# Performance work log

Hardware: AMD Instinct MI355X
Metric: run time of the kernel (lower is better)

The kernel has to match this reference:

```python
import jax, jax.numpy as jnp
import numpy as np

B, L, N, C = 32, 12, 2048, 3
D = 64          # embed_dim
TOPK = 8
NK = 16         # n_kernel
TOD = 288
DOW = 7
OUT = 12        # output_len
NLAYER = 3
HS = 3 * D + TOPK * D + D        # spatial_hidden_dim = 768
HT = 4 * D + TOPK * D + D        # temporal_hidden_dim = 832
HC = int(100 * 0.1 * np.log(N / 0.1))  # EmbeddingTrainer bottleneck = 99
EPS = 1e-8


def setup_inputs() -> dict:
    key = jax.random.key(0)
    ks = jax.random.split(key, 20)
    r = lambda i, shape, s=0.02: jax.random.normal(ks[i], shape, jnp.float32) * s
    return dict(
        history_data=jax.random.uniform(ks[0], (B, L, N, C), jnp.float32),
        future_data=jax.random.uniform(ks[1], (B, OUT, N, C), jnp.float32),
        node_emb=r(2, (N, D), 0.1),
        et_w1=r(3, (HC, N)), et_b1=jnp.zeros((HC,), jnp.float32),
        et_w2=r(4, (N, HC)), et_b2=jnp.zeros((N,), jnp.float32),
        tod_emb=r(5, (TOD, D), 0.1), dow_emb=r(6, (DOW, D), 0.1),
        ts_w=r(7, (D, L), 0.1),
        feature_emb=r(8, (NK, D), 0.1),
        kernels=r(9, (NK, L), 0.1),
        sp_w=r(10, (D, HS)), sp_b=jnp.zeros((D,), jnp.float32),
        mlp_w1=r(11, (NLAYER, HT, HT), 0.01), mlp_b1=jnp.zeros((NLAYER, HT), jnp.float32),
        mlp_w2=r(12, (NLAYER, HT, HT), 0.01), mlp_b2=jnp.zeros((NLAYER, HT), jnp.float32),
        treg_w=r(13, (OUT, L), 0.1), treg_b=jnp.zeros((OUT,), jnp.float32),
        sreg_w=r(14, (OUT, HT), 0.02), sreg_b=jnp.zeros((OUT,), jnp.float32),
        daily_data=r(15, (TOD, N), 0.01), weekly_data=r(16, (DOW, N), 0.01),
        w_spatial=jnp.full((N,), 0.5, jnp.float32),
        batch_seen=0, epoch=0, train=1,
    )


def _forward(history_data, future_data, node_emb, et_w1, et_b1, et_w2, et_b2,
             tod_emb, dow_emb, ts_w, feature_emb, kernels, sp_w, sp_b,
             mlp_w1, mlp_b1, mlp_w2, mlp_b2, treg_w, treg_b, sreg_w, sreg_b,
             daily_data, weekly_data, w_spatial):
    x_in = history_data[..., 0]                              # (B,L,N)
    # --- temporal embeddings at last step ---
    tod_idx = (history_data[:, -1, :, 1] * TOD).astype(jnp.int32)   # (B,N)
    dow_idx = (history_data[:, -1, :, 2] * DOW).astype(jnp.int32)
    tid = tod_emb[tod_idx]                                   # (B,N,D)
    diw = dow_emb[dow_idx]
    # --- time-series embedding (1x1 conv over L channels) ---
    ts_emb = jnp.einsum('bln,dl->bdn', x_in, ts_w)           # (B,D,N)
    # --- EmbeddingTrainer: compress/reconstruct along node axis ---
    z = jax.nn.relu(jnp.einsum('nd,hn->dh', node_emb, et_w1) + et_b1)   # (D,HC)
    proj_node = (jnp.einsum('dh,nh->dn', z, et_w2) + et_b2).T           # (N,D)
    # --- NFConnection: cosine correlation node-series vs kernel bank ---
    xn = x_in / (jnp.linalg.norm(x_in, axis=1, keepdims=True) + EPS)
    kn = kernels / (jnp.linalg.norm(kernels, axis=1, keepdims=True) + EPS)
    conn = jnp.einsum('bln,kl->bnk', xn, kn)                 # (B,N,NK)
    c_weight, c_index = jax.lax.top_k(conn, TOPK)            # (B,N,TOPK)
    corr = jax.nn.sigmoid(c_weight)[..., None] * feature_emb[c_index]   # (B,N,TOPK,D)
    corr_ch = corr.reshape(B, N, TOPK * D).transpose(0, 2, 1)           # (B,TOPK*D,N)
    Hinc = jax.nn.one_hot(c_index, NK, dtype=jnp.float32).sum(axis=2)   # (B,N,NK)
    # --- assemble spatial encoder input ---
    node_ch = jnp.broadcast_to(proj_node.T[None], (B, D, N))
    enc_in = jnp.concatenate([ts_emb, node_ch, tid.transpose(0, 2, 1),
                              diw.transpose(0, 2, 1), corr_ch], axis=1)  # (B,HS,N)
    # --- SpatiaEncoder: 1x1 proj + hypergraph message passing ---
    h0 = jax.nn.relu(jnp.einsum('bcn,dc->bdn', enc_in, sp_w) + sp_b[None, :, None])
    deg_e = jnp.maximum(Hinc.sum(axis=1), 1.0)               # (B,NK)
    edge = jnp.einsum('bnk,bdn->bdk', Hinc, h0) / deg_e[:, None, :]
    edge = edge + feature_emb.T[None]                        # add hyperedge (kernel) embeddings
    msg = jnp.einsum('bnk,bdk->bdn', Hinc, edge) / TOPK
    sp_out = h0 + msg + proj_node.T[None]                    # (B,D,N)
    # --- temporal encoder: residual MLP stack ---
    h = jnp.concatenate([enc_in, sp_out], axis=1)            # (B,HT,N)
    for i in range(NLAYER):
        z1 = jax.nn.relu(jnp.einsum('bcn,dc->bdn', h, mlp_w1[i]) + mlp_b1[i][None, :, None])
        h = h + jnp.einsum('bcn,dc->bdn', z1, mlp_w2[i]) + mlp_b2[i][None, :, None]
    forecast_sp = jnp.einsum('bcn,oc->bon', h, sreg_w) + sreg_b[None, :, None]  # (B,OUT,N)
    # --- temporal branch: RevIN + daily/weekly cycle queues ---
    di_b = (history_data[:, :, 0, 1] * TOD).astype(jnp.int32)   # (B,L)
    wi_b = (history_data[:, :, 0, 2] * DOW).astype(jnp.int32)
    mean = x_in.mean(axis=1, keepdims=True)                  # (B,1,N)
    var = jnp.var(x_in, axis=1, keepdims=True, ddof=1) + 1e-5
    xr = (x_in - mean) / jnp.sqrt(var) - (daily_data[di_b] + weekly_data[wi_b])
    forecast_t = jnp.einsum('bln,ol->bon', xr, treg_w) + treg_b[None, :, None]
    di_f = (future_data[:, :, 0, 1] * TOD).astype(jnp.int32)
    wi_f = (future_data[:, :, 0, 2] * DOW).astype(jnp.int32)
    forecast_t = forecast_t + daily_data[di_f] + weekly_data[wi_f]
    forecast_t = forecast_t * jnp.sqrt(var) + mean
    pred = w_spatial[None, None, :] * forecast_sp + (1.0 - w_spatial)[None, None, :] * forecast_t
    return pred[..., None]                                   # (B,OUT,N,1)


def reference(history_data, future_data, node_emb, et_w1, et_b1, et_w2, et_b2,
              tod_emb, dow_emb, ts_w, feature_emb, kernels, sp_w, sp_b,
              mlp_w1, mlp_b1, mlp_w2, mlp_b2, treg_w, treg_b, sreg_w, sreg_b,
              daily_data, weekly_data, w_spatial, batch_seen, epoch, train):
    return _forward(history_data, future_data, node_emb, et_w1, et_b1, et_w2, et_b2,
                    tod_emb, dow_emb, ts_w, feature_emb, kernels, sp_w, sp_b,
                    mlp_w1, mlp_b1, mlp_w2, mlp_b2, treg_w, treg_b, sreg_w, sreg_b,
                    daily_data, weekly_data, w_spatial)
```

## Files before the change

### kernel.cpp

```cpp
#include <hip/hip_runtime.h>
#include <hip/hip_bf16.h>
#include <math.h>

#define BB 32
#define LL 12
#define NN 2048
#define DD 64
#define TOPK 8
#define NKER 16
#define OUTL 12
#define HS 768
#define HT 832
#define HTP 896
#define HCB 99
#define BN (BB*NN)

typedef __attribute__((ext_vector_type(8))) short bf16x8;
typedef __attribute__((ext_vector_type(4))) float f32x4;

#define GLOAD16(gp, lp) __builtin_amdgcn_global_load_lds( \
    (const __attribute__((address_space(1))) unsigned int*)(uintptr_t)(gp), \
    (__attribute__((address_space(3))) unsigned int*)(unsigned int)(uintptr_t)(lp), \
    16, 0, 0)

__global__ __launch_bounds__(256)
void f2b_pad_kernel(const float* __restrict__ x, __hip_bfloat16* __restrict__ y,
                    int rows, int cols, int prows) {
    int i = blockIdx.x * 256 + threadIdx.x;
    if (i >= prows * cols) return;
    int r = i / cols;
    y[i] = __float2bfloat16((r < rows) ? x[i] : 0.f);
}

__global__ __launch_bounds__(64)
void et_z_kernel(const float* __restrict__ node_emb, const float* __restrict__ w1,
                 const float* __restrict__ b1, float* __restrict__ z) {
    int hh = blockIdx.x;
    int d  = threadIdx.x;
    float acc = 0.f;
    for (int nn = 0; nn < NN; ++nn)
        acc += node_emb[nn*DD + d] * w1[(size_t)hh*NN + nn];
    acc += b1[hh];
    z[d*HCB + hh] = fmaxf(acc, 0.f);
}

__global__ __launch_bounds__(64)
void et_proj_kernel(const float* __restrict__ z, const float* __restrict__ w2,
                    const float* __restrict__ b2, float* __restrict__ proj) {
    int nn = blockIdx.x;
    int d  = threadIdx.x;
    float acc = 0.f;
    for (int hh = 0; hh < HCB; ++hh)
        acc += z[d*HCB + hh] * w2[nn*HCB + hh];
    proj[nn*DD + d] = acc + b2[nn];
}

__global__ __launch_bounds__(64)
void prep_kernel(const float* __restrict__ hist, const float* __restrict__ proj,
                 const float* __restrict__ tod_emb, const float* __restrict__ dow_emb,
                 const float* __restrict__ ts_w, const float* __restrict__ feat_emb,
                 const float* __restrict__ kern, __hip_bfloat16* __restrict__ h,
                 int* __restrict__ cidx, unsigned int* __restrict__ mask) {
    const int tok = blockIdx.x;
    const int b = tok >> 11, n = tok & (NN-1);
    const int lane = threadIdx.x;
    __shared__ float xs[LL];
    __shared__ float conn_s[NKER];
    __shared__ int   idx_s[TOPK];
    __shared__ float w_s[TOPK];

    if (lane < LL)
        xs[lane] = hist[((size_t)(b*LL + lane) * NN + n) * 3];
    __syncthreads();

    if (lane < NKER) {
        float xn = 0.f;
        #pragma unroll
        for (int l = 0; l < LL; ++l) xn += xs[l]*xs[l];
        xn = sqrtf(xn) + 1e-8f;
        float kn = 0.f;
        #pragma unroll
        for (int l = 0; l < LL; ++l) { float kv = kern[lane*LL + l]; kn += kv*kv; }
        kn = sqrtf(kn) + 1e-8f;
        float dot = 0.f;
        #pragma unroll
        for (int l = 0; l < LL; ++l) dot += (xs[l]/xn) * (kern[lane*LL + l]/kn);
        conn_s[lane] = dot;
    }
    __syncthreads();

    if (lane == 0) {
        float c[NKER];
        #pragma unroll
        for (int k = 0; k < NKER; ++k) c[k] = conn_s[k];
        unsigned int mk = 0;
        for (int j = 0; j < TOPK; ++j) {
            float best = -1e30f; int bi = 0;
            #pragma unroll
            for (int k = 0; k < NKER; ++k)
                if (c[k] > best) { best = c[k]; bi = k; }
            idx_s[j] = bi;
            w_s[j] = 1.f / (1.f + expf(-best));
            c[bi] = -1e30f;
            mk |= (1u << bi);
            cidx[(size_t)tok*TOPK + j] = bi;
        }
        mask[tok] = mk;
    }
    __syncthreads();

    const int d = lane;
    float ts = 0.f;
    #pragma unroll
    for (int l = 0; l < LL; ++l) ts += xs[l] * ts_w[d*LL + l];
    size_t base = (size_t)tok * HT;
    h[base + d] = __float2bfloat16(ts);
    h[base + DD + d] = __float2bfloat16(proj[n*DD + d]);
    size_t last = ((size_t)(b*LL + (LL-1)) * NN + n) * 3;
    int ti = (int)(hist[last + 1] * 288.f);
    int wi = (int)(hist[last + 2] * 7.f);
    h[base + 2*DD + d] = __float2bfloat16(tod_emb[ti*DD + d]);
    h[base + 3*DD + d] = __float2bfloat16(dow_emb[wi*DD + d]);
    #pragma unroll
    for (int j = 0; j < TOPK; ++j)
        h[base + 4*DD + j*DD + d] = __float2bfloat16(w_s[j] * feat_emb[idx_s[j]*DD + d]);
}

template<int RELU, int ACCUM, int CF32, int NCOLS>
__global__ __launch_bounds__(256)
void gemm128(const unsigned short* __restrict__ A, int lda,
             const unsigned short* __restrict__ W, int ldb,
             const float* __restrict__ bias,
             void* __restrict__ Cp, int ldc, int K, int ntiles) {
    __shared__ __align__(16) unsigned short As[128*64];
    __shared__ __align__(16) unsigned short Bs[128*64];

    int nwg = gridDim.x, bid = blockIdx.x;
    int q = nwg >> 3, r = nwg & 7;
    int xcd = bid & 7, idx = bid >> 3;
    int swz = ((xcd < r) ? xcd*(q+1) : r*(q+1) + (xcd-r)*q) + idx;
    const long long m0 = (long long)(swz / ntiles) * 128;
    const int n0 = (swz % ntiles) * 128;

    const int tid = threadIdx.x;
    const int wave = tid >> 6, lane = tid & 63;
    const int wr = wave >> 1, wc = wave & 1;
    const int l15 = lane & 15, l4 = lane >> 4;

    const int srow = tid >> 3;
    const int gc = ((tid & 7) ^ ((tid >> 3) & 7)) * 8;
    const unsigned short* ag = A + (m0 + srow) * (long long)lda + gc;
    const unsigned short* bg = W + (long long)(n0 + srow) * ldb + gc;

    f32x4 acc[4][4] = {};

    for (int k0 = 0; k0 < K; k0 += 64) {
        #pragma unroll
        for (int qq = 0; qq < 4; ++qq) {
            GLOAD16(ag + k0 + (long long)qq*32*lda, &As[(qq*256 + tid)*8]);
            GLOAD16(bg + k0 + (long long)qq*32*ldb, &Bs[(qq*256 + tid)*8]);
        }
        __syncthreads();
        #pragma unroll
        for (int kh = 0; kh < 2; ++kh) {
            bf16x8 af[4], bf[4];
            #pragma unroll
            for (int i = 0; i < 4; ++i) {
                int ra = wr*64 + i*16 + l15;
                af[i] = *(const bf16x8*)&As[ra*64 + (((kh*4 + l4) ^ (ra & 7)) * 8)];
            }
            #pragma unroll
            for (int j = 0; j < 4; ++j) {
                int rb = wc*64 + j*16 + l15;
                bf[j] = *(const bf16x8*)&Bs[rb*64 + (((kh*4 + l4) ^ (rb & 7)) * 8)];
            }
            #pragma unroll
            for (int i = 0; i < 4; ++i)
                #pragma unroll
                for (int j = 0; j < 4; ++j)
                    acc[i][j] = __builtin_amdgcn_mfma_f32_16x16x32_bf16(af[i], bf[j], acc[i][j], 0, 0, 0);
        }
        __syncthreads();
    }

    float* Cf = (float*)Cp;
    __hip_bfloat16* Cb = (__hip_bfloat16*)Cp;
    #pragma unroll
    for (int i = 0; i < 4; ++i) {
        #pragma unroll
        for (int j = 0; j < 4; ++j) {
            int col = n0 + wc*64 + j*16 + l15;
            if (col < NCOLS) {
                float bv = bias[col];
                #pragma unroll
                for (int rg = 0; rg < 4; ++rg) {
                    long long row = m0 + wr*64 + i*16 + l4*4 + rg;
                    float v = acc[i][j][rg] + bv;
                    if (RELU) v = fmaxf(v, 0.f);
                    if (CF32) {
                        Cf[row*ldc + col] = v;
                    } else {
                        if (ACCUM) v += __bfloat162float(Cb[row*ldc + col]);
                        Cb[row*ldc + col] = __float2bfloat16(v);
                    }
                }
            }
        }
    }
}

__global__ __launch_bounds__(256)
void edge_kernel(const float* __restrict__ h0, const unsigned int* __restrict__ mask,
                 const float* __restrict__ feat_emb, float* __restrict__ edge) {
    int b = blockIdx.x >> 4, k = blockIdx.x & 15;
    int g = threadIdx.x >> 6, d = threadIdx.x & 63;
    __shared__ float accs[4][64];
    __shared__ int cnts[4];
    float acc = 0.f; int cnt = 0;
    size_t tb = (size_t)b * NN;
    #pragma unroll 4
    for (int nn = g; nn < NN; nn += 4) {
        unsigned int bit = (mask[tb + nn] >> k) & 1u;
        acc += (float)bit * h0[(tb + nn)*DD + d];
        cnt += (int)bit;
    }
    accs[g][d] = acc;
    if (d == 0) cnts[g] = cnt;
    __syncthreads();
    if (g == 0) {
        float a = accs[0][d] + accs[1][d] + accs[2][d] + accs[3][d];
        int c = cnts[0] + cnts[1] + cnts[2] + cnts[3];
        edge[((size_t)b*NKER + k)*DD + d] = a / fmaxf((float)c, 1.f) + feat_emb[k*DD + d];
    }
}

__global__ __launch_bounds__(256)
void msg_kernel(const float* __restrict__ h0, const float* __restrict__ edge,
                const int* __restrict__ cidx, const float* __restrict__ proj,
                __hip_bfloat16* __restrict__ h) {
    __shared__ float eS[NKER*DD];
    int t0 = blockIdx.x * 4;
    int b = t0 >> 11;
    for (int i = threadIdx.x; i < NKER*DD; i += 256) eS[i] = edge[(size_t)b*NKER*DD + i];
    __syncthreads();
    int g = threadIdx.x >> 6, lane = threadIdx.x & 63;
    int tok = t0 + g, n = tok & (NN-1);
    float m = 0.f;
    #pragma unroll
    for (int j = 0; j < TOPK; ++j)
        m += eS[cidx[(size_t)tok*TOPK + j]*DD + lane];
    float sp = h0[(size_t)tok*DD + lane] + m*0.125f + proj[n*DD + lane];
    h[(size_t)tok*HT + HS + lane] = __float2bfloat16(sp);
}

__global__ __launch_bounds__(256)
void temporal_kernel(const float* __restrict__ hist, const float* __restrict__ fut,
                     const float* __restrict__ daily, const float* __restrict__ weekly,
                     const float* __restrict__ treg_w, const float* __restrict__ treg_b,
                     float* __restrict__ outp) {
    __shared__ int s_di[LL], s_wi[LL], s_df[OUTL], s_wf[OUTL];
    __shared__ float s_tw[OUTL*LL], s_tb[OUTL];
    int tid = threadIdx.x;
    int tok = blockIdx.x * 256 + tid;
    int b = tok >> 11, n = tok & (NN-1);
    if (tid < LL) {
        size_t hb = ((size_t)(b*LL + tid) * NN) * 3;
        s_di[tid] = (int)(hist[hb + 1] * 288.f);
        s_wi[tid] = (int)(hist[hb + 2] * 7.f);
        size_t fb = ((size_t)(b*OUTL + tid) * NN) * 3;
        s_df[tid] = (int)(fut[fb + 1] * 288.f);
        s_wf[tid] = (int)(fut[fb + 2] * 7.f);
        s_tb[tid] = treg_b[tid];
    }
    if (tid < OUTL*LL) s_tw[tid] = treg_w[tid];
    __syncthreads();
    float x[LL];
    float mean = 0.f;
    #pragma unroll
    for (int l = 0; l < LL; ++l) {
        x[l] = hist[((size_t)(b*LL + l) * NN + n) * 3];
        mean += x[l];
    }
    mean *= (1.f/12.f);
    float ss = 0.f;
    #pragma unroll
    for (int l = 0; l < LL; ++l) { float dd = x[l]-mean; ss += dd*dd; }
    float sd = sqrtf(ss*(1.f/11.f) + 1e-5f);
    float xr[LL];
    #pragma unroll
    for (int l = 0; l < LL; ++l)
        xr[l] = (x[l]-mean)/sd - daily[(size_t)s_di[l]*NN + n] - weekly[(size_t)s_wi[l]*NN + n];
    #pragma unroll
    for (int o = 0; o < OUTL; ++o) {
        float f = s_tb[o];
        #pragma unroll
        for (int l = 0; l < LL; ++l) f += xr[l]*s_tw[o*LL + l];
        f += daily[(size_t)s_df[o]*NN + n] + weekly[(size_t)s_wf[o]*NN + n];
        f = f*sd + mean;
        outp[((size_t)b*OUTL + o)*NN + n] = f;
    }
}

__global__ __launch_bounds__(256)
void final_kernel(const __hip_bfloat16* __restrict__ h, const float* __restrict__ sreg_w,
                  const float* __restrict__ sreg_b, const float* __restrict__ w_sp,
                  float* __restrict__ outp) {
    int g = threadIdx.x >> 6, lane = threadIdx.x & 63;
    int tok = blockIdx.x*4 + g;
    int b = tok >> 11, n = tok & (NN-1);
    float acc[OUTL];
    #pragma unroll
    for (int o = 0; o < OUTL; ++o) acc[o] = 0.f;
    size_t base = (size_t)tok * HT;
    for (int c = lane; c < HT; c += 64) {
        float hv = __bfloat162float(h[base + c]);
        #pragma unroll
        for (int o = 0; o < OUTL; ++o) acc[o] += hv * sreg_w[o*HT + c];
    }
    #pragma unroll
    for (int o = 0; o < OUTL; ++o) {
        #pragma unroll
        for (int s = 32; s >= 1; s >>= 1)
            acc[o] += __shfl_xor(acc[o], s, 64);
    }
    float v = 0.f;
    #pragma unroll
    for (int o = 0; o < OUTL; ++o) if (lane == o) v = acc[o] + sreg_b[o];
    if (lane < OUTL) {
        size_t oi = ((size_t)b*OUTL + lane)*NN + n;
        float t = outp[oi];
        float w = w_sp[n];
        outp[oi] = w*v + (1.f-w)*t;
    }
}

extern "C" void kernel_launch(void* const* d_in, const int* in_sizes, int n_in,
                              void* d_out, int out_size, void* d_ws, size_t ws_size,
                              hipStream_t stream) {
    const float* hist    = (const float*)d_in[0];
    const float* fut     = (const float*)d_in[1];
    const float* node_emb= (const float*)d_in[2];
    const float* et_w1   = (const float*)d_in[3];
    const float* et_b1   = (const float*)d_in[4];
    const float* et_w2   = (const float*)d_in[5];
    const float* et_b2   = (const float*)d_in[6];
    const float* tod_emb = (const float*)d_in[7];
    const float* dow_emb = (const float*)d_in[8];
    const float* ts_w    = (const float*)d_in[9];
    const float* feat    = (const float*)d_in[10];
    const float* kern    = (const float*)d_in[11];
    const float* sp_w    = (const float*)d_in[12];
    const float* sp_b    = (const float*)d_in[13];
    const float* mlp_w1  = (const float*)d_in[14];
    const float* mlp_b1  = (const float*)d_in[15];
    const float* mlp_w2  = (const float*)d_in[16];
    const float* mlp_b2  = (const float*)d_in[17];
    const float* treg_w  = (const float*)d_in[18];
    const float* treg_b  = (const float*)d_in[19];
    const float* sreg_w  = (const float*)d_in[20];
    const float* sreg_b  = (const float*)d_in[21];
    const float* daily   = (const float*)d_in[22];
    const float* weekly  = (const float*)d_in[23];
    const float* w_sp    = (const float*)d_in[24];
    float* out = (float*)d_out;

    char* ws = (char*)d_ws;
    __hip_bfloat16* h    = (__hip_bfloat16*)(ws);
    float*          h0   = (float*)(ws + 109051904ULL);
    float*          proj = (float*)(ws + 125829120ULL);
    float*          zet  = (float*)(ws + 126353408ULL);
    float*          edge = (float*)(ws + 126386176ULL);
    int*            cidx = (int*)  (ws + 126517248ULL);
    unsigned int*   mask = (unsigned int*)(ws + 128614400ULL);
    __hip_bfloat16* spwb = (__hip_bfloat16*)(ws + 128876544ULL);
    __hip_bfloat16* w1b  = (__hip_bfloat16*)(ws + 129073152ULL);
    __hip_bfloat16* w2b  = (__hip_bfloat16*)(ws + 133545984ULL);
    const size_t z1_off = 138018816ULL;
    __hip_bfloat16* z1   = (__hip_bfloat16*)(ws + z1_off);

    long long avail = (ws_size > z1_off) ? (long long)(ws_size - z1_off) : 0;
    long long chunk = (avail / (HT*2)) & ~127LL;
    if (chunk > BN) chunk = BN;
    if (chunk < 128) chunk = 128;

    f2b_pad_kernel<<<(128*HS + 255)/256, 256, 0, stream>>>(sp_w, spwb, 64, HS, 128);
    for (int i = 0; i < 3; ++i) {
        f2b_pad_kernel<<<(HTP*HT + 255)/256, 256, 0, stream>>>(
            mlp_w1 + (size_t)i*HT*HT, w1b + (size_t)i*HTP*HT, HT, HT, HTP);
        f2b_pad_kernel<<<(HTP*HT + 255)/256, 256, 0, stream>>>(
            mlp_w2 + (size_t)i*HT*HT, w2b + (size_t)i*HTP*HT, HT, HT, HTP);
    }

    et_z_kernel  <<<HCB, 64, 0, stream>>>(node_emb, et_w1, et_b1, zet);
    et_proj_kernel<<<NN, 64, 0, stream>>>(zet, et_w2, et_b2, proj);
    prep_kernel  <<<BN, 64, 0, stream>>>(hist, proj, tod_emb, dow_emb, ts_w, feat, kern,
                                         h, cidx, mask);
    gemm128<1,0,1,64><<<BN/128, 256, 0, stream>>>(
        (const unsigned short*)h, HT, (const unsigned short*)spwb, HS, sp_b, h0, DD, HS, 1);
    edge_kernel  <<<BB*NKER, 256, 0, stream>>>(h0, mask, feat, edge);
    msg_kernel   <<<BN/4, 256, 0, stream>>>(h0, edge, cidx, proj, h);
    for (int i = 0; i < 3; ++i) {
        for (long long ms = 0; ms < BN; ms += chunk) {
            long long mm = (BN - ms < chunk) ? (BN - ms) : chunk;
            int grid = (int)(mm/128) * (HTP/128);
            gemm128<1,0,0,HT><<<grid, 256, 0, stream>>>(
                (const unsigned short*)(h + ms*HT), HT,
                (const unsigned short*)(w1b + (size_t)i*HTP*HT), HT,
                mlp_b1 + i*HT, z1, HT, HT, HTP/128);
            gemm128<0,1,0,HT><<<grid, 256, 0, stream>>>(
                (const unsigned short*)z1, HT,
                (const unsigned short*)(w2b + (size_t)i*HTP*HT), HT,
                mlp_b2 + i*HT, h + ms*HT, HT, HT, HTP/128);
        }
    }
    temporal_kernel<<<BN/256, 256, 0, stream>>>(hist, fut, daily, weekly, treg_w, treg_b, out);
    final_kernel <<<BN/4, 256, 0, stream>>>(h, sreg_w, sreg_b, w_sp, out);
}
```

Before: 1.217 ms.

## Use double-buffered 256x256 tile GEMM for the temporal MLP layers

Adds a 512-thread gemm256 kernel with 256x256 output tiles and a two-stage LDS double buffer. It uses explicit vmcnt waits so the next K-slice loads while the MFMAs run on the current one. The six MLP GEMMs switch to it, with weights padded to 1024 rows, and the chunk size is aligned to 256. The aim is more data reuse per tile and less exposed global-load latency, at the cost of about 19% wasted MFMA work on padded columns (832 of 1024) and a 128KB LDS footprint that likely limits each CU to one workgroup.

After: 1.333 ms. 9.5% more time.

```diff
diff --git a/kernel.cpp b/kernel.cpp
--- a/kernel.cpp
+++ b/kernel.cpp
@@ -11,7 +11,7 @@
 #define OUTL 12
 #define HS 768
 #define HT 832
-#define HTP 896
+#define HTP2 1024
 #define HCB 99
 #define BN (BB*NN)
 
@@ -126,12 +126,114 @@
         h[base + 4*DD + j*DD + d] = __float2bfloat16(w_s[j] * feat_emb[idx_s[j]*DD + d]);
 }
 
-template<int RELU, int ACCUM, int CF32, int NCOLS>
+
+__device__ __forceinline__
+void g256_stage(const unsigned short* ag, const unsigned short* bg,
+                long long lda, long long ldb, int k0,
+                unsigned short* As, unsigned short* Bs, int tid) {
+    #pragma unroll
+    for (int qq = 0; qq < 4; ++qq) {
+        GLOAD16(ag + k0 + (long long)(qq*64)*lda, &As[(qq*512 + tid)*8]);
+        GLOAD16(bg + k0 + (long long)(qq*64)*ldb, &Bs[(qq*512 + tid)*8]);
+    }
+}
+
+__device__ __forceinline__
+void g256_compute(const unsigned short* As, const unsigned short* Bs,
+                  int wr, int wc, int l15, int l4, f32x4 acc[8][4]) {
+    #pragma unroll
+    for (int ks = 0; ks < 2; ++ks) {
+        bf16x8 af[8], bf[4];
+        #pragma unroll
+        for (int i = 0; i < 8; ++i) {
+            int ra = wr*128 + i*16 + l15;
+            af[i] = *(const bf16x8*)&As[ra*64 + (((ks*4 + l4) ^ (ra & 7)) * 8)];
+        }
+        #pragma unroll
+        for (int j = 0; j < 4; ++j) {
+            int rb = wc*64 + j*16 + l15;
+            bf[j] = *(const bf16x8*)&Bs[rb*64 + (((ks*4 + l4) ^ (rb & 7)) * 8)];
+        }
+        #pragma unroll
+        for (int i = 0; i < 8; ++i)
+            #pragma unroll
+            for (int j = 0; j < 4; ++j)
+                acc[i][j] = __builtin_amdgcn_mfma_f32_16x16x32_bf16(af[i], bf[j], acc[i][j], 0, 0, 0);
+    }
+}
+
+template<int RELU, int ACCUM, int NCOLS>
+__global__ __launch_bounds__(512, 2)
+void gemm256(const unsigned short* __restrict__ A, int lda,
+             const unsigned short* __restrict__ W, int ldb,
+             const float* __restrict__ bias,
+             __hip_bfloat16* __restrict__ C, int ldc, int K, int ntiles) {
+    __shared__ __align__(16) unsigned short As[2*256*64];
+    __shared__ __align__(16) unsigned short Bs[2*256*64];
+
+    int nwg = gridDim.x, bid = blockIdx.x;
+    int q = nwg >> 3, r = nwg & 7;
+    int xcd = bid & 7, idx = bid >> 3;
+    int swz = ((xcd < r) ? xcd*(q+1) : r*(q+1) + (xcd-r)*q) + idx;
+    const long long m0 = (long long)(swz / ntiles) * 256;
+    const int n0 = (swz % ntiles) * 256;
+
+    const int tid = threadIdx.x;
+    const int wave = tid >> 6, lane = tid & 63;
+    const int wr = wave >> 2, wc = wave & 3;
+    const int l15 = lane & 15, l4 = lane >> 4;
+
+    const int srow = tid >> 3;
+    const int gc = ((tid & 7) ^ ((tid >> 3) & 7)) * 8;
+    const unsigned short* ag = A + (m0 + srow) * (long long)lda + gc;
+    const unsigned short* bg = W + (long long)(n0 + srow) * ldb + gc;
+
+    f32x4 acc[8][4] = {};
+    const int NT = K >> 6;
+
+    g256_stage(ag, bg, lda, ldb, 0, As, Bs, tid);
+    if (NT > 1) g256_stage(ag, bg, lda, ldb, 64, As + 256*64, Bs + 256*64, tid);
+
+    for (int t = 0; t < NT; ++t) {
+        if (t + 1 < NT) { asm volatile("s_waitcnt vmcnt(8)" ::: "memory"); }
+        else            { asm volatile("s_waitcnt vmcnt(0)" ::: "memory"); }
+        __builtin_amdgcn_s_barrier();
+        __builtin_amdgcn_sched_barrier(0);
+        const int buf = t & 1;
+        g256_compute(As + buf*256*64, Bs + buf*256*64, wr, wc, l15, l4, acc);
+        __builtin_amdgcn_sched_barrier(0);
+        __builtin_amdgcn_s_barrier();
+        __builtin_amdgcn_sched_barrier(0);
+        if (t + 2 < NT)
+            g256_stage(ag, bg, lda, ldb, (t+2) << 6, As + buf*256*64, Bs + buf*256*64, tid);
+    }
+
+    #pragma unroll
+    for (int i = 0; i < 8; ++i) {
+        #pragma unroll
+        for (int j = 0; j < 4; ++j) {
+            int col = n0 + wc*64 + j*16 + l15;
+            if (col < NCOLS) {
+                float bv = bias[col];
+                #pragma unroll
+                for (int rg = 0; rg < 4; ++rg) {
+                    long long row = m0 + wr*128 + i*16 + l4*4 + rg;
+                    float v = acc[i][j][rg] + bv;
+                    if (RELU) v = fmaxf(v, 0.f);
+                    if (ACCUM) v += __bfloat162float(C[row*ldc + col]);
+                    C[row*ldc + col] = __float2bfloat16(v);
+                }
+            }
+        }
+    }
+}
+
+template<int RELU, int NCOLS>
 __global__ __launch_bounds__(256)
 void gemm128(const unsigned short* __restrict__ A, int lda,
              const unsigned short* __restrict__ W, int ldb,
              const float* __restrict__ bias,
-             void* __restrict__ Cp, int ldc, int K, int ntiles) {
+             float* __restrict__ C, int ldc, int K, int ntiles) {
     __shared__ __align__(16) unsigned short As[128*64];
     __shared__ __align__(16) unsigned short Bs[128*64];
 
@@ -157,8 +259,8 @@
     for (int k0 = 0; k0 < K; k0 += 64) {
         #pragma unroll
         for (int qq = 0; qq < 4; ++qq) {
-            GLOAD16(ag + k0 + (long long)qq*32*lda, &As[(qq*256 + tid)*8]);
-            GLOAD16(bg + k0 + (long long)qq*32*ldb, &Bs[(qq*256 + tid)*8]);
+            GLOAD16(ag + k0 + (long long)(qq*32)*lda, &As[(qq*256 + tid)*8]);
+            GLOAD16(bg + k0 + (long long)(qq*32)*ldb, &Bs[(qq*256 + tid)*8]);
         }
         __syncthreads();
         #pragma unroll
@@ -183,8 +285,6 @@
         __syncthreads();
     }
 
-    float* Cf = (float*)Cp;
-    __hip_bfloat16* Cb = (__hip_bfloat16*)Cp;
     #pragma unroll
     for (int i = 0; i < 4; ++i) {
         #pragma unroll
@@ -197,12 +297,7 @@
                     long long row = m0 + wr*64 + i*16 + l4*4 + rg;
                     float v = acc[i][j][rg] + bv;
                     if (RELU) v = fmaxf(v, 0.f);
-                    if (CF32) {
-                        Cf[row*ldc + col] = v;
-                    } else {
-                        if (ACCUM) v += __bfloat162float(Cb[row*ldc + col]);
-                        Cb[row*ldc + col] = __float2bfloat16(v);
-                    }
+                    C[row*ldc + col] = v;
                 }
             }
         }
@@ -374,43 +469,43 @@
     unsigned int*   mask = (unsigned int*)(ws + 128614400ULL);
     __hip_bfloat16* spwb = (__hip_bfloat16*)(ws + 128876544ULL);
     __hip_bfloat16* w1b  = (__hip_bfloat16*)(ws + 129073152ULL);
-    __hip_bfloat16* w2b  = (__hip_bfloat16*)(ws + 133545984ULL);
-    const size_t z1_off = 138018816ULL;
+    __hip_bfloat16* w2b  = (__hip_bfloat16*)(ws + 134184960ULL);
+    const size_t z1_off = 139296768ULL;
     __hip_bfloat16* z1   = (__hip_bfloat16*)(ws + z1_off);
 
     long long avail = (ws_size > z1_off) ? (long long)(ws_size - z1_off) : 0;
-    long long chunk = (avail / (HT*2)) & ~127LL;
+    long long chunk = (avail / (HT*2)) & ~255LL;
     if (chunk > BN) chunk = BN;
-    if (chunk < 128) chunk = 128;
+    if (chunk < 256) chunk = 256;
 
     f2b_pad_kernel<<<(128*HS + 255)/256, 256, 0, stream>>>(sp_w, spwb, 64, HS, 128);
     for (int i = 0; i < 3; ++i) {
-        f2b_pad_kernel<<<(HTP*HT + 255)/256, 256, 0, stream>>>(
-            mlp_w1 + (size_t)i*HT*HT, w1b + (size_t)i*HTP*HT, HT, HT, HTP);
-        f2b_pad_kernel<<<(HTP*HT + 255)/256, 256, 0, stream>>>(
-            mlp_w2 + (size_t)i*HT*HT, w2b + (size_t)i*HTP*HT, HT, HT, HTP);
+        f2b_pad_kernel<<<(HTP2*HT + 255)/256, 256, 0, stream>>>(
+            mlp_w1 + (size_t)i*HT*HT, w1b + (size_t)i*HTP2*HT, HT, HT, HTP2);
+        f2b_pad_kernel<<<(HTP2*HT + 255)/256, 256, 0, stream>>>(
+            mlp_w2 + (size_t)i*HT*HT, w2b + (size_t)i*HTP2*HT, HT, HT, HTP2);
     }
 
     et_z_kernel  <<<HCB, 64, 0, stream>>>(node_emb, et_w1, et_b1, zet);
     et_proj_kernel<<<NN, 64, 0, stream>>>(zet, et_w2, et_b2, proj);
     prep_kernel  <<<BN, 64, 0, stream>>>(hist, proj, tod_emb, dow_emb, ts_w, feat, kern,
                                          h, cidx, mask);
-    gemm128<1,0,1,64><<<BN/128, 256, 0, stream>>>(
+    gemm128<1,64><<<BN/128, 256, 0, stream>>>(
         (const unsigned short*)h, HT, (const unsigned short*)spwb, HS, sp_b, h0, DD, HS, 1);
     edge_kernel  <<<BB*NKER, 256, 0, stream>>>(h0, mask, feat, edge);
     msg_kernel   <<<BN/4, 256, 0, stream>>>(h0, edge, cidx, proj, h);
     for (int i = 0; i < 3; ++i) {
         for (long long ms = 0; ms < BN; ms += chunk) {
             long long mm = (BN - ms < chunk) ? (BN - ms) : chunk;
-            int grid = (int)(mm/128) * (HTP/128);
-            gemm128<1,0,0,HT><<<grid, 256, 0, stream>>>(
+            int grid = (int)(mm/256) * (HTP2/256);
+            gemm256<1,0,HT><<<grid, 512, 0, stream>>>(
                 (const unsigned short*)(h + ms*HT), HT,
-                (const unsigned short*)(w1b + (size_t)i*HTP*HT), HT,
-                mlp_b1 + i*HT, z1, HT, HT, HTP/128);
-            gemm128<0,1,0,HT><<<grid, 256, 0, stream>>>(
+                (const unsigned short*)(w1b + (size_t)i*HTP2*HT), HT,
+                mlp_b1 + i*HT, z1, HT, HT, HTP2/256);
+            gemm256<0,1,HT><<<grid, 512, 0, stream>>>(
                 (const unsigned short*)z1, HT,
-                (const unsigned short*)(w2b + (size_t)i*HTP*HT), HT,
-                mlp_b2 + i*HT, h + ms*HT, HT, HT, HTP/128);
+                (const unsigned short*)(w2b + (size_t)i*HTP2*HT), HT,
+                mlp_b2 + i*HT, h + ms*HT, HT, HT, HTP2/256);
         }
     }
     temporal_kernel<<<BN/256, 256, 0, stream>>>(hist, fut, daily, weekly, treg_w, treg_b, out);
```
